# Performance work log

Hardware: AMD Instinct MI355X
Metric: run time of the kernel (lower is better)

## Reference

```python
import jax, jax.numpy as jnp
import numpy as np

D_MODEL = 512
N_HEADS = 8
D_K = 64
D_V = 64
SCALE = 1.0 / np.sqrt(D_K).astype(np.float32)
LN_EPS = 1e-5


def setup_inputs() -> dict:
    key = jax.random.key(0)
    ks = jax.random.split(key, 8)
    B, S = 4, 2048
    xavier = np.sqrt(6.0 / (D_MODEL + D_MODEL)).astype(np.float32)
    return {
        "input_Q": jax.random.normal(ks[0], (B, S, D_MODEL), jnp.float32),
        "input_K": jax.random.normal(ks[1], (B, S, D_MODEL), jnp.float32),
        "input_V": jax.random.normal(ks[2], (B, S, D_MODEL), jnp.float32),
        "attn_mask": jax.random.randint(ks[3], (B, S, S), 0, 2).astype(bool),
        "W_Q": jax.random.uniform(ks[4], (D_MODEL, D_MODEL), jnp.float32, -xavier, xavier),
        "W_K": jax.random.uniform(ks[5], (D_MODEL, D_MODEL), jnp.float32, -xavier, xavier),
        "W_V": jax.random.uniform(ks[6], (D_MODEL, D_MODEL), jnp.float32, -xavier, xavier),
        "W_fc": jax.random.uniform(ks[7], (D_MODEL, D_MODEL), jnp.float32, -xavier, xavier),
        "ln_gamma": jnp.ones((D_MODEL,), jnp.float32),
        "ln_beta": jnp.zeros((D_MODEL,), jnp.float32),
    }


def _layernorm(x, gamma, beta):
    mu = jnp.mean(x, axis=-1, keepdims=True)
    var = jnp.mean(jnp.square(x - mu), axis=-1, keepdims=True)
    return (x - mu) * jax.lax.rsqrt(var + LN_EPS) * gamma + beta


def reference(input_Q, input_K, input_V, attn_mask, W_Q, W_K, W_V, W_fc, ln_gamma, ln_beta):
    B = input_Q.shape[0]
    # torch Linear: x @ W.T ; W is (out, in)
    def proj(x, W):
        y = jnp.einsum('bsd,ed->bse', x, W)  # (B,S,n_heads*d_k)
        return y.reshape(B, -1, N_HEADS, D_K).transpose(0, 2, 1, 3)  # (B,H,S,dk)

    Q = proj(input_Q, W_Q)
    K = proj(input_K, W_K)
    V = proj(input_V, W_V)

    scores = jnp.einsum('bhqd,bhkd->bhqk', Q, K) * SCALE
    scores = jnp.clip(scores, -1e9, 1e10)
    mask = attn_mask[:, None, :, :]  # broadcast over heads
    scores = jnp.where(mask, jnp.float32(-1e9), scores)
    attn = jax.nn.softmax(scores, axis=-1)
    attn = jnp.clip(attn, 1e-8, 1.0)
    result = jnp.einsum('bhqk,bhkd->bhqd', attn, V)
    result = result.transpose(0, 2, 1, 3).reshape(B, -1, N_HEADS * D_V)
    output = jnp.einsum('bsd,ed->bse', result, W_fc)
    out = _layernorm(output + input_Q, ln_gamma, ln_beta)
    return (out, attn)
```

## Files before the change

kernel.cpp:

```cpp
#include <hip/hip_runtime.h>

typedef float  f32x4  __attribute__((ext_vector_type(4)));
typedef __bf16 bf16x8 __attribute__((ext_vector_type(8)));

#define MFMA_BF16(a, b, c) __builtin_amdgcn_mfma_f32_16x16x32_bf16((a), (b), (c), 0, 0, 0)

#define BDIM   4
#define SEQ    2048
#define DM     512
#define NH     8
#define DK     64
#define KT     64
#define NT     (SEQ / KT)
#define QB     128
#define PS     72
#define KTDK   (KT * DK)
#define C2LOG2E  0.18033688011112042f
#define MASKED_X (-115.41560327111707f)

static __device__ __forceinline__ unsigned short f2bf(float f) {
  unsigned int u = __builtin_bit_cast(unsigned int, f);
  u += 0x7fffu + ((u >> 16) & 1u);
  return (unsigned short)(u >> 16);
}
static __device__ __forceinline__ unsigned short rhu(float f) {
  unsigned int u = __builtin_bit_cast(unsigned int, f);
  return (unsigned short)((u + 0x8000u) >> 16);
}
static __device__ __forceinline__ float bf2f(unsigned short u) {
  return __builtin_bit_cast(float, (unsigned)u << 16);
}
static __device__ __forceinline__ float exp2_fast(float x) {
  float r;
  asm("v_exp_f32 %0, %1" : "=v"(r) : "v"(x));
  return r;
}
static __device__ __forceinline__ float log2_fast(float x) {
  float r;
  asm("v_log_f32 %0, %1" : "=v"(r) : "v"(x));
  return r;
}
static __device__ __forceinline__ void gload16(const void* g, unsigned short* l) {
  __builtin_amdgcn_global_load_lds((const __attribute__((address_space(1))) void*)g,
                                   (__attribute__((address_space(3))) void*)l, 16, 0, 0);
}
static __device__ __forceinline__ bf16x8 lds128(const unsigned short* base, int row, int m) {
  return *(const bf16x8*)((const char*)base + row * 128 + (((m) ^ (row & 7)) << 4));
}

__global__ __launch_bounds__(256) void cvt7_kernel(
    const float* __restrict__ x0, const float* __restrict__ x1, const float* __restrict__ x2,
    const float* __restrict__ w0, const float* __restrict__ w1, const float* __restrict__ w2,
    const float* __restrict__ w3,
    unsigned short* __restrict__ dx0, unsigned short* __restrict__ dx1,
    unsigned short* __restrict__ dx2, unsigned short* __restrict__ dw0,
    unsigned short* __restrict__ dw1, unsigned short* __restrict__ dw2,
    unsigned short* __restrict__ dw3, int nx4, int nw4) {
  const int z = blockIdx.y;
  const float* src;
  unsigned short* dst;
  int n4;
  switch (z) {
    case 0: src = x0; dst = dx0; n4 = nx4; break;
    case 1: src = x1; dst = dx1; n4 = nx4; break;
    case 2: src = x2; dst = dx2; n4 = nx4; break;
    case 3: src = w0; dst = dw0; n4 = nw4; break;
    case 4: src = w1; dst = dw1; n4 = nw4; break;
    case 5: src = w2; dst = dw2; n4 = nw4; break;
    default: src = w3; dst = dw3; n4 = nw4; break;
  }
  int i = blockIdx.x * 256 + threadIdx.x;
  if (i >= n4) return;
  float4 v = reinterpret_cast<const float4*>(src)[i];
  ushort4 o;
  o.x = f2bf(v.x); o.y = f2bf(v.y); o.z = f2bf(v.z); o.w = f2bf(v.w);
  reinterpret_cast<ushort4*>(dst)[i] = o;
}

__global__ void detect_mask_kernel(const unsigned int* __restrict__ m, int* __restrict__ flag) {
  __shared__ int s;
  if (threadIdx.x == 0) s = 0;
  __syncthreads();
  int any = 0;
  for (int i = threadIdx.x; i < 4096; i += 256) any |= (m[i] > 1u) ? 1 : 0;
  if (any) atomicOr(&s, 1);
  __syncthreads();
  if (threadIdx.x == 0) *flag = s;
}

__global__ __launch_bounds__(256) void mask_pack_kernel(const unsigned char* __restrict__ m8,
                                                        const int* __restrict__ m32,
                                                        const int* __restrict__ flag,
                                                        unsigned long long* __restrict__ bits) {
  const int wid = blockIdx.x * 256 + threadIdx.x;
  const int use8 = *flag;
  unsigned long long v = 0;
  if (use8) {
    const uchar4* p = (const uchar4*)(m8 + (size_t)wid * 64);
#pragma unroll
    for (int c = 0; c < 16; ++c) {
      uchar4 q = p[c];
      v |= ((unsigned long long)(q.x != 0)) << (c * 4 + 0);
      v |= ((unsigned long long)(q.y != 0)) << (c * 4 + 1);
      v |= ((unsigned long long)(q.z != 0)) << (c * 4 + 2);
      v |= ((unsigned long long)(q.w != 0)) << (c * 4 + 3);
    }
  } else {
    const int4* p = (const int4*)(m32 + (size_t)wid * 64);
#pragma unroll
    for (int c = 0; c < 16; ++c) {
      int4 q = p[c];
      v |= ((unsigned long long)(q.x != 0)) << (c * 4 + 0);
      v |= ((unsigned long long)(q.y != 0)) << (c * 4 + 1);
      v |= ((unsigned long long)(q.z != 0)) << (c * 4 + 2);
      v |= ((unsigned long long)(q.w != 0)) << (c * 4 + 3);
    }
  }
  bits[wid] = v;
}

__device__ __forceinline__ void gemm128_main(const unsigned short* __restrict__ A,
                                             const unsigned short* __restrict__ B,
                                             int K, int row0, int col0,
                                             unsigned short* lds, f32x4 acc[4][4]) {
  const int tid  = threadIdx.x;
  const int w    = tid >> 6;
  const int lane = tid & 63;
  const int lr   = lane & 15;
  const int lk   = (lane >> 4) << 3;
  const int wm   = (w >> 1) << 6;
  const int wn   = (w & 1) << 6;
  unsigned short* As = lds;
  unsigned short* Bs = lds + 128 * 32;
  const int r0 = tid >> 2;
  const int c0 = (tid & 3) << 3;
  const unsigned short* a0 = A + (size_t)(row0 + r0) * K + c0;
  const unsigned short* a1 = A + (size_t)(row0 + r0 + 64) * K + c0;
  const unsigned short* b0 = B + (size_t)(col0 + r0) * K + c0;
  const unsigned short* b1 = B + (size_t)(col0 + r0 + 64) * K + c0;
  unsigned short* dA0 = &As[tid * 8];
  unsigned short* dA1 = &As[(tid + 256) * 8];
  unsigned short* dB0 = &Bs[tid * 8];
  unsigned short* dB1 = &Bs[(tid + 256) * 8];
  for (int k0 = 0; k0 < K; k0 += 32) {
    __syncthreads();
    gload16(a0 + k0, dA0);
    gload16(a1 + k0, dA1);
    gload16(b0 + k0, dB0);
    gload16(b1 + k0, dB1);
    __syncthreads();
    bf16x8 af[4], bfr[4];
#pragma unroll
    for (int mi = 0; mi < 4; ++mi) af[mi]  = *(const bf16x8*)&As[(wm + mi * 16 + lr) * 32 + lk];
#pragma unroll
    for (int ni = 0; ni < 4; ++ni) bfr[ni] = *(const bf16x8*)&Bs[(wn + ni * 16 + lr) * 32 + lk];
#pragma unroll
    for (int mi = 0; mi < 4; ++mi)
#pragma unroll
      for (int ni = 0; ni < 4; ++ni)
        acc[mi][ni] = MFMA_BF16(af[mi], bfr[ni], acc[mi][ni]);
  }
}

__global__ __launch_bounds__(256) void proj_kernel(
    const unsigned short* __restrict__ Xq, const unsigned short* __restrict__ Xk,
    const unsigned short* __restrict__ Xv,
    const unsigned short* __restrict__ Wq, const unsigned short* __restrict__ Wk,
    const unsigned short* __restrict__ Wv,
    unsigned short* __restrict__ Qh, unsigned short* __restrict__ Kh,
    unsigned short* __restrict__ VT) {
  __shared__ __align__(16) unsigned short lds[2 * 128 * 32];
  const int z = blockIdx.z;
  const unsigned short* A = (z == 0) ? Xq : ((z == 1) ? Xk : Xv);
  const unsigned short* B = (z == 0) ? Wq : ((z == 1) ? Wk : Wv);
  unsigned short* O       = (z == 0) ? Qh : ((z == 1) ? Kh : VT);
  const int row0 = blockIdx.x * 128, col0 = blockIdx.y * 128;
  f32x4 acc[4][4];
  const f32x4 zero = {0.f, 0.f, 0.f, 0.f};
#pragma unroll
  for (int mi = 0; mi < 4; ++mi)
#pragma unroll
    for (int ni = 0; ni < 4; ++ni) acc[mi][ni] = zero;
  gemm128_main(A, B, DM, row0, col0, lds, acc);
  const int w = threadIdx.x >> 6, lane = threadIdx.x & 63;
  const int lr = lane & 15, lg = lane >> 4;
  const int wm = (w >> 1) << 6, wn = (w & 1) << 6;
#pragma unroll
  for (int mi = 0; mi < 4; ++mi)
#pragma unroll
    for (int ni = 0; ni < 4; ++ni)
#pragma unroll
      for (int j = 0; j < 4; ++j) {
        const int m = row0 + wm + mi * 16 + lg * 4 + j;
        const int n = col0 + wn + ni * 16 + lr;
        const int b = m >> 11, s = m & 2047;
        const int h = n >> 6,  d = n & 63;
        const unsigned short val = f2bf(acc[mi][ni][j]);
        if (z == 2)
          O[(((size_t)(b * NH + h)) * DK + d) * SEQ + s] = val;
        else
          O[(((size_t)(b * NH + h)) * SEQ + s) * DK + d] = val;
      }
}

__global__ __launch_bounds__(256) void fc_kernel(const unsigned short* __restrict__ A,
                                                 const unsigned short* __restrict__ W,
                                                 float* __restrict__ Out) {
  __shared__ __align__(16) unsigned short lds[2 * 128 * 32];
  const int row0 = blockIdx.x * 128, col0 = blockIdx.y * 128;
  f32x4 acc[4][4];
  const f32x4 zero = {0.f, 0.f, 0.f, 0.f};
#pragma unroll
  for (int mi = 0; mi < 4; ++mi)
#pragma unroll
    for (int ni = 0; ni < 4; ++ni) acc[mi][ni] = zero;
  gemm128_main(A, W, DM, row0, col0, lds, acc);
  const int w = threadIdx.x >> 6, lane = threadIdx.x & 63;
  const int lr = lane & 15, lg = lane >> 4;
  const int wm = (w >> 1) << 6, wn = (w & 1) << 6;
#pragma unroll
  for (int mi = 0; mi < 4; ++mi)
#pragma unroll
    for (int ni = 0; ni < 4; ++ni)
#pragma unroll
      for (int j = 0; j < 4; ++j) {
        const int m = row0 + wm + mi * 16 + lg * 4 + j;
        const int n = col0 + wn + ni * 16 + lr;
        Out[(size_t)m * DM + n] = acc[mi][ni][j];
      }
}

__global__ __launch_bounds__(512, 4) void attn_kernel(
    const unsigned short* __restrict__ Qh, const unsigned short* __restrict__ Kh,
    const unsigned short* __restrict__ VT, const unsigned long long* __restrict__ Mb,
    float* __restrict__ attn_out, unsigned short* __restrict__ R16) {
  __shared__ __align__(16) unsigned short Ks[2][KTDK];
  __shared__ __align__(16) unsigned short Vs[2][KTDK];
  __shared__ __align__(16) unsigned short Pl[8][16 * PS];
  const int id  = blockIdx.x + 16 * (blockIdx.y + 8 * blockIdx.z);
  const int q8  = id >> 3;
  const int bh  = (id & 7) * 4 + (q8 >> 4);
  const int qt  = q8 & 15;
  const int b   = bh >> 3;
  const int tid = threadIdx.x, w = tid >> 6, lane = tid & 63;
  const int lr = lane & 15, lg = lane >> 4;
  const unsigned short* Qp = Qh + (size_t)bh * SEQ * DK;
  const unsigned short* Kp = Kh + (size_t)bh * SEQ * DK;
  const unsigned short* Vp = VT + (size_t)bh * DK * SEQ;
  float* ap = attn_out + (size_t)bh * SEQ * SEQ;

  const int qb = qt * QB + w * 16;
  const bf16x8 qf0 = *(const bf16x8*)(Qp + (size_t)(qb + lr) * DK + lg * 8);
  const bf16x8 qf1 = *(const bf16x8*)(Qp + (size_t)(qb + lr) * DK + 32 + lg * 8);
  const unsigned long long* mrow = Mb + ((size_t)b * SEQ + qb + lr) * 32;

  const int srow = tid >> 3, schunk = tid & 7;
  const int sg = schunk ^ (srow & 7);
  const unsigned short* kstage = Kp + (size_t)srow * DK + sg * 8;
  const unsigned short* vstage = Vp + (size_t)srow * SEQ + sg * 8;
  unsigned short* kdst0 = &Ks[0][tid * 8];
  unsigned short* kdst1 = &Ks[1][tid * 8];
  unsigned short* vdst0 = &Vs[0][tid * 8];
  unsigned short* vdst1 = &Vs[1][tid * 8];

  float l2 = 0.f;
  gload16(kstage, kdst0);
  __syncthreads();
  for (int t = 0; t < NT; ++t) {
    const unsigned short* Kb = Ks[t & 1];
    if (t + 1 < NT) gload16(kstage + (size_t)(t + 1) * KTDK, (t & 1) ? kdst0 : kdst1);
    const unsigned long long mr = mrow[t];
#pragma unroll
    for (int ni = 0; ni < 4; ++ni) {
      const int r = ni * 16 + lr;
      bf16x8 k0 = lds128(Kb, r, lg);
      bf16x8 k1 = lds128(Kb, r, lg + 4);
      f32x4 z = {0.f, 0.f, 0.f, 0.f};
      z = MFMA_BF16(k0, qf0, z);
      z = MFMA_BF16(k1, qf1, z);
#pragma unroll
      for (int j = 0; j < 4; ++j) {
        const float t1 = z[j] * C2LOG2E;
        const float x = ((mr >> (ni * 16 + lg * 4 + j)) & 1ull) ? MASKED_X : t1;
        l2 += exp2_fast(x);
      }
    }
    __syncthreads();
  }
  l2 += __shfl_xor(l2, 16);
  l2 += __shfl_xor(l2, 32);
  const float negllog = -log2_fast(l2);
  const float mAlt = MASKED_X + negllog;

  f32x4 o[4];
  const f32x4 zero = {0.f, 0.f, 0.f, 0.f};
#pragma unroll
  for (int nd = 0; nd < 4; ++nd) o[nd] = zero;
  unsigned short* Pw = &Pl[w][0];

  gload16(kstage, kdst0);
  gload16(vstage, vdst0);
  asm volatile("s_waitcnt vmcnt(0)" ::: "memory");
  __builtin_amdgcn_s_barrier();
  for (int t = 0; t < NT; ++t) {
    const unsigned short* Kb = Ks[t & 1];
    const unsigned short* Vb = Vs[t & 1];
    if (t + 1 < NT) {
      gload16(kstage + (size_t)(t + 1) * KTDK, (t & 1) ? kdst0 : kdst1);
      gload16(vstage + (size_t)(t + 1) * KT,   (t & 1) ? vdst0 : vdst1);
    }
    const unsigned long long mr = mrow[t];
#pragma unroll
    for (int ni = 0; ni < 4; ++ni) {
      const int r = ni * 16 + lr;
      bf16x8 k0 = lds128(Kb, r, lg);
      bf16x8 k1 = lds128(Kb, r, lg + 4);
      f32x4 z = {0.f, 0.f, 0.f, 0.f};
      z = MFMA_BF16(k0, qf0, z);
      z = MFMA_BF16(k1, qf1, z);
      float p[4];
#pragma unroll
      for (int j = 0; j < 4; ++j) {
        const float t1 = fmaf(z[j], C2LOG2E, negllog);
        const float x = ((mr >> (ni * 16 + lg * 4 + j)) & 1ull) ? mAlt : t1;
        p[j] = exp2_fast(x);
      }
      ushort4 pk = {rhu(p[0]), rhu(p[1]), rhu(p[2]), rhu(p[3])};
      *(ushort4*)&Pw[lr * PS + ni * 16 + lg * 4] = pk;
    }
    const bf16x8 pf0 = *(const bf16x8*)&Pw[lr * PS + lg * 8];
    const bf16x8 pf1 = *(const bf16x8*)&Pw[lr * PS + 32 + lg * 8];
#pragma unroll
    for (int nd = 0; nd < 4; ++nd) {
      const int r = nd * 16 + lr;
      o[nd] = MFMA_BF16(pf0, lds128(Vb, r, lg), o[nd]);
    }
#pragma unroll
    for (int nd = 0; nd < 4; ++nd) {
      const int r = nd * 16 + lr;
      o[nd] = MFMA_BF16(pf1, lds128(Vb, r, lg + 4), o[nd]);
    }
#pragma unroll
    for (int j = 0; j < 4; ++j) {
      const int r = lg * 4 + j;
      ushort4 pk = *(const ushort4*)&Pw[r * PS + lr * 4];
      float4 f = {bf2f(pk.x), bf2f(pk.y), bf2f(pk.z), bf2f(pk.w)};
      *(float4*)(ap + (size_t)(qb + r) * SEQ + t * KT + lr * 4) = f;
    }
    if (t + 1 < NT) {
      asm volatile("s_waitcnt vmcnt(4)" ::: "memory");
      __builtin_amdgcn_s_barrier();
    }
  }
#pragma unroll
  for (int nd = 0; nd < 4; ++nd)
#pragma unroll
    for (int j = 0; j < 4; ++j)
      R16[((size_t)(b * SEQ + qb + lg * 4 + j)) * DM + (bh & 7) * DK + nd * 16 + lr] = f2bf(o[nd][j]);
}

__global__ __launch_bounds__(256) void ln_kernel(const float* __restrict__ fc,
                                                 const float* __restrict__ xq,
                                                 const float* __restrict__ gamma,
                                                 const float* __restrict__ beta,
                                                 float* __restrict__ out) {
  const int row = blockIdx.x * 4 + (threadIdx.x >> 6);
  const int lane = threadIdx.x & 63;
  const float* f = fc + (size_t)row * DM;
  const float* x = xq + (size_t)row * DM;
  float v[8];
  float s = 0.f, ss = 0.f;
#pragma unroll
  for (int i = 0; i < 8; ++i) {
    const int c = lane + i * 64;
    const float t = f[c] + x[c];
    v[i] = t; s += t; ss += t * t;
  }
#pragma unroll
  for (int off = 1; off < 64; off <<= 1) {
    s  += __shfl_xor(s, off);
    ss += __shfl_xor(ss, off);
  }
  const float mu  = s * (1.f / 512.f);
  const float var = ss * (1.f / 512.f) - mu * mu;
  const float inv = rsqrtf(var + 1e-5f);
  float* op = out + (size_t)row * DM;
#pragma unroll
  for (int i = 0; i < 8; ++i) {
    const int c = lane + i * 64;
    op[c] = (v[i] - mu) * inv * gamma[c] + beta[c];
  }
}


extern "C" void kernel_launch(void* const* d_in, const int* in_sizes, int n_in,
                              void* d_out, int out_size, void* d_ws, size_t ws_size,
                              hipStream_t stream) {
  const float* xq   = (const float*)d_in[0];
  const float* xk   = (const float*)d_in[1];
  const float* xv   = (const float*)d_in[2];
  const void*  mask = d_in[3];
  const float* wq   = (const float*)d_in[4];
  const float* wk   = (const float*)d_in[5];
  const float* wv   = (const float*)d_in[6];
  const float* wfc  = (const float*)d_in[7];
  const float* gamma = (const float*)d_in[8];
  const float* beta  = (const float*)d_in[9];

  float* out = (float*)d_out;
  float* attn_out = out + (size_t)BDIM * SEQ * DM;

  char* ws = (char*)d_ws;
  unsigned short* XQ16 = (unsigned short*)(ws);
  unsigned short* XK16 = (unsigned short*)(ws + 8388608);
  unsigned short* XV16 = (unsigned short*)(ws + 16777216);
  unsigned short* WQ16 = (unsigned short*)(ws + 25165824);
  unsigned short* WK16 = (unsigned short*)(ws + 25690112);
  unsigned short* WV16 = (unsigned short*)(ws + 26214400);
  unsigned short* WF16 = (unsigned short*)(ws + 26738688);
  unsigned short* Qh   = (unsigned short*)(ws + 27262976);
  unsigned short* Kh   = (unsigned short*)(ws + 35651584);
  unsigned short* VT   = (unsigned short*)(ws + 44040192);
  unsigned long long* Mbits = (unsigned long long*)(ws);
  unsigned short* R16  = (unsigned short*)(ws + 16777216);
  float*          FC32 = (float*)(ws + 27262976);
  int*            FLAG = (int*)(ws + 52428800);

  const int NX4 = BDIM * SEQ * DM / 4;
  const int NW4 = DM * DM / 4;

  detect_mask_kernel<<<1, 256, 0, stream>>>((const unsigned int*)mask, FLAG);
  cvt7_kernel<<<dim3(NX4 / 256, 7), 256, 0, stream>>>(xq, xk, xv, wq, wk, wv, wfc,
                                                      XQ16, XK16, XV16,
                                                      WQ16, WK16, WV16, WF16, NX4, NW4);
  proj_kernel<<<dim3(64, 4, 3), 256, 0, stream>>>(XQ16, XK16, XV16,
                                                  WQ16, WK16, WV16, Qh, Kh, VT);
  mask_pack_kernel<<<1024, 256, 0, stream>>>((const unsigned char*)mask,
                                             (const int*)mask, FLAG, Mbits);
  attn_kernel<<<dim3(16, NH, BDIM), 512, 0, stream>>>(Qh, Kh, VT, Mbits, attn_out, R16);
  fc_kernel<<<dim3(64, 4, 1), 256, 0, stream>>>(R16, WF16, FC32);
  ln_kernel<<<2048, 256, 0, stream>>>(FC32, xq, gamma, beta, out);
}
```

Measured before the change: 305.0 us.

## Give each attention wave two query row tiles to reuse K/V LDS fragments

The attention block shrinks from 8 waves to 4, and each wave now handles two 16-row query tiles (A and B). Every K and V fragment read from LDS feeds two MFMAs, so LDS reads per MFMA are halved. Each thread stages two 16-byte chunks per tile, and the vmcnt wait goes from 4 to 8 to match the extra loads. In exchange, registers per wave roughly double and there are fewer waves per block to hide latency, with launch bounds set to 256 threads and 3 blocks per CU.

```diff
diff --git a/kernel.cpp b/kernel.cpp
--- a/kernel.cpp
+++ b/kernel.cpp
@@ -230,13 +230,13 @@
       }
 }
 
-__global__ __launch_bounds__(512, 4) void attn_kernel(
+__global__ __launch_bounds__(256, 3) void attn_kernel(
     const unsigned short* __restrict__ Qh, const unsigned short* __restrict__ Kh,
     const unsigned short* __restrict__ VT, const unsigned long long* __restrict__ Mb,
     float* __restrict__ attn_out, unsigned short* __restrict__ R16) {
   __shared__ __align__(16) unsigned short Ks[2][KTDK];
   __shared__ __align__(16) unsigned short Vs[2][KTDK];
-  __shared__ __align__(16) unsigned short Pl[8][16 * PS];
+  __shared__ __align__(16) unsigned short Pl[4][2][16 * PS];
   const int id  = blockIdx.x + 16 * (blockIdx.y + 8 * blockIdx.z);
   const int q8  = id >> 3;
   const int bh  = (id & 7) * 4 + (q8 >> 4);
@@ -249,114 +249,151 @@
   const unsigned short* Vp = VT + (size_t)bh * DK * SEQ;
   float* ap = attn_out + (size_t)bh * SEQ * SEQ;
 
-  const int qb = qt * QB + w * 16;
-  const bf16x8 qf0 = *(const bf16x8*)(Qp + (size_t)(qb + lr) * DK + lg * 8);
-  const bf16x8 qf1 = *(const bf16x8*)(Qp + (size_t)(qb + lr) * DK + 32 + lg * 8);
-  const unsigned long long* mrow = Mb + ((size_t)b * SEQ + qb + lr) * 32;
-
-  const int srow = tid >> 3, schunk = tid & 7;
-  const int sg = schunk ^ (srow & 7);
-  const unsigned short* kstage = Kp + (size_t)srow * DK + sg * 8;
-  const unsigned short* vstage = Vp + (size_t)srow * SEQ + sg * 8;
-  unsigned short* kdst0 = &Ks[0][tid * 8];
-  unsigned short* kdst1 = &Ks[1][tid * 8];
-  unsigned short* vdst0 = &Vs[0][tid * 8];
-  unsigned short* vdst1 = &Vs[1][tid * 8];
-
-  float l2 = 0.f;
-  gload16(kstage, kdst0);
+  const int qbA = qt * QB + w * 32;
+  const int qbB = qbA + 16;
+  const bf16x8 qfA0 = *(const bf16x8*)(Qp + (size_t)(qbA + lr) * DK + lg * 8);
+  const bf16x8 qfA1 = *(const bf16x8*)(Qp + (size_t)(qbA + lr) * DK + 32 + lg * 8);
+  const bf16x8 qfB0 = *(const bf16x8*)(Qp + (size_t)(qbB + lr) * DK + lg * 8);
+  const bf16x8 qfB1 = *(const bf16x8*)(Qp + (size_t)(qbB + lr) * DK + 32 + lg * 8);
+  const unsigned long long* mrowA = Mb + ((size_t)b * SEQ + qbA + lr) * 32;
+  const unsigned long long* mrowB = Mb + ((size_t)b * SEQ + qbB + lr) * 32;
+
+  const int ci0 = tid, ci1 = tid + 256;
+  const int sr0 = ci0 >> 3, sc0 = (ci0 & 7) ^ (sr0 & 7);
+  const int sr1 = ci1 >> 3, sc1 = (ci1 & 7) ^ (sr1 & 7);
+  const unsigned short* kst0 = Kp + (size_t)sr0 * DK + sc0 * 8;
+  const unsigned short* kst1 = Kp + (size_t)sr1 * DK + sc1 * 8;
+  const unsigned short* vst0 = Vp + (size_t)sr0 * SEQ + sc0 * 8;
+  const unsigned short* vst1 = Vp + (size_t)sr1 * SEQ + sc1 * 8;
+
+  float l2A = 0.f, l2B = 0.f;
+  gload16(kst0, &Ks[0][ci0 * 8]);
+  gload16(kst1, &Ks[0][ci1 * 8]);
   __syncthreads();
   for (int t = 0; t < NT; ++t) {
     const unsigned short* Kb = Ks[t & 1];
-    if (t + 1 < NT) gload16(kstage + (size_t)(t + 1) * KTDK, (t & 1) ? kdst0 : kdst1);
-    const unsigned long long mr = mrow[t];
+    if (t + 1 < NT) {
+      gload16(kst0 + (size_t)(t + 1) * KTDK, &Ks[(t & 1) ^ 1][ci0 * 8]);
+      gload16(kst1 + (size_t)(t + 1) * KTDK, &Ks[(t & 1) ^ 1][ci1 * 8]);
+    }
+    const unsigned long long mrA = mrowA[t];
+    const unsigned long long mrB = mrowB[t];
 #pragma unroll
     for (int ni = 0; ni < 4; ++ni) {
       const int r = ni * 16 + lr;
       bf16x8 k0 = lds128(Kb, r, lg);
       bf16x8 k1 = lds128(Kb, r, lg + 4);
-      f32x4 z = {0.f, 0.f, 0.f, 0.f};
-      z = MFMA_BF16(k0, qf0, z);
-      z = MFMA_BF16(k1, qf1, z);
+      f32x4 zA = {0.f, 0.f, 0.f, 0.f};
+      zA = MFMA_BF16(k0, qfA0, zA);
+      zA = MFMA_BF16(k1, qfA1, zA);
+      f32x4 zB = {0.f, 0.f, 0.f, 0.f};
+      zB = MFMA_BF16(k0, qfB0, zB);
+      zB = MFMA_BF16(k1, qfB1, zB);
 #pragma unroll
       for (int j = 0; j < 4; ++j) {
-        const float t1 = z[j] * C2LOG2E;
-        const float x = ((mr >> (ni * 16 + lg * 4 + j)) & 1ull) ? MASKED_X : t1;
-        l2 += exp2_fast(x);
+        const int bit = ni * 16 + lg * 4 + j;
+        const float xA = ((mrA >> bit) & 1ull) ? MASKED_X : zA[j] * C2LOG2E;
+        const float xB = ((mrB >> bit) & 1ull) ? MASKED_X : zB[j] * C2LOG2E;
+        l2A += exp2_fast(xA);
+        l2B += exp2_fast(xB);
       }
     }
     __syncthreads();
   }
-  l2 += __shfl_xor(l2, 16);
-  l2 += __shfl_xor(l2, 32);
-  const float negllog = -log2_fast(l2);
-  const float mAlt = MASKED_X + negllog;
-
-  f32x4 o[4];
+  l2A += __shfl_xor(l2A, 16);
+  l2A += __shfl_xor(l2A, 32);
+  l2B += __shfl_xor(l2B, 16);
+  l2B += __shfl_xor(l2B, 32);
+  const float negllogA = -log2_fast(l2A);
+  const float negllogB = -log2_fast(l2B);
+  const float mAltA = MASKED_X + negllogA;
+  const float mAltB = MASKED_X + negllogB;
+
+  f32x4 oA[4], oB[4];
   const f32x4 zero = {0.f, 0.f, 0.f, 0.f};
 #pragma unroll
-  for (int nd = 0; nd < 4; ++nd) o[nd] = zero;
-  unsigned short* Pw = &Pl[w][0];
-
-  gload16(kstage, kdst0);
-  gload16(vstage, vdst0);
+  for (int nd = 0; nd < 4; ++nd) { oA[nd] = zero; oB[nd] = zero; }
+  unsigned short* PwA = &Pl[w][0][0];
+  unsigned short* PwB = &Pl[w][1][0];
+
+  gload16(kst0, &Ks[0][ci0 * 8]);
+  gload16(kst1, &Ks[0][ci1 * 8]);
+  gload16(vst0, &Vs[0][ci0 * 8]);
+  gload16(vst1, &Vs[0][ci1 * 8]);
   asm volatile("s_waitcnt vmcnt(0)" ::: "memory");
   __builtin_amdgcn_s_barrier();
   for (int t = 0; t < NT; ++t) {
     const unsigned short* Kb = Ks[t & 1];
     const unsigned short* Vb = Vs[t & 1];
     if (t + 1 < NT) {
-      gload16(kstage + (size_t)(t + 1) * KTDK, (t & 1) ? kdst0 : kdst1);
-      gload16(vstage + (size_t)(t + 1) * KT,   (t & 1) ? vdst0 : vdst1);
-    }
-    const unsigned long long mr = mrow[t];
+      gload16(kst0 + (size_t)(t + 1) * KTDK, &Ks[(t & 1) ^ 1][ci0 * 8]);
+      gload16(kst1 + (size_t)(t + 1) * KTDK, &Ks[(t & 1) ^ 1][ci1 * 8]);
+      gload16(vst0 + (size_t)(t + 1) * KT,   &Vs[(t & 1) ^ 1][ci0 * 8]);
+      gload16(vst1 + (size_t)(t + 1) * KT,   &Vs[(t & 1) ^ 1][ci1 * 8]);
+    }
+    const unsigned long long mrA = mrowA[t];
+    const unsigned long long mrB = mrowB[t];
 #pragma unroll
     for (int ni = 0; ni < 4; ++ni) {
       const int r = ni * 16 + lr;
       bf16x8 k0 = lds128(Kb, r, lg);
       bf16x8 k1 = lds128(Kb, r, lg + 4);
-      f32x4 z = {0.f, 0.f, 0.f, 0.f};
-      z = MFMA_BF16(k0, qf0, z);
-      z = MFMA_BF16(k1, qf1, z);
-      float p[4];
+      f32x4 zA = {0.f, 0.f, 0.f, 0.f};
+      zA = MFMA_BF16(k0, qfA0, zA);
+      zA = MFMA_BF16(k1, qfA1, zA);
+      f32x4 zB = {0.f, 0.f, 0.f, 0.f};
+      zB = MFMA_BF16(k0, qfB0, zB);
+      zB = MFMA_BF16(k1, qfB1, zB);
+      float pA[4], pB[4];
 #pragma unroll
       for (int j = 0; j < 4; ++j) {
-        const float t1 = fmaf(z[j], C2LOG2E, negllog);
-        const float x = ((mr >> (ni * 16 + lg * 4 + j)) & 1ull) ? mAlt : t1;
-        p[j] = exp2_fast(x);
+        const int bit = ni * 16 + lg * 4 + j;
+        const float xA = ((mrA >> bit) & 1ull) ? mAltA : fmaf(zA[j], C2LOG2E, negllogA);
+        const float xB = ((mrB >> bit) & 1ull) ? mAltB : fmaf(zB[j], C2LOG2E, negllogB);
+        pA[j] = exp2_fast(xA);
+        pB[j] = exp2_fast(xB);
       }
-      ushort4 pk = {rhu(p[0]), rhu(p[1]), rhu(p[2]), rhu(p[3])};
-      *(ushort4*)&Pw[lr * PS + ni * 16 + lg * 4] = pk;
-    }
-    const bf16x8 pf0 = *(const bf16x8*)&Pw[lr * PS + lg * 8];
-    const bf16x8 pf1 = *(const bf16x8*)&Pw[lr * PS + 32 + lg * 8];
+      ushort4 pkA = {rhu(pA[0]), rhu(pA[1]), rhu(pA[2]), rhu(pA[3])};
+      ushort4 pkB = {rhu(pB[0]), rhu(pB[1]), rhu(pB[2]), rhu(pB[3])};
+      *(ushort4*)&PwA[lr * PS + ni * 16 + lg * 4] = pkA;
+      *(ushort4*)&PwB[lr * PS + ni * 16 + lg * 4] = pkB;
+    }
+    const bf16x8 pfA0 = *(const bf16x8*)&PwA[lr * PS + lg * 8];
+    const bf16x8 pfA1 = *(const bf16x8*)&PwA[lr * PS + 32 + lg * 8];
+    const bf16x8 pfB0 = *(const bf16x8*)&PwB[lr * PS + lg * 8];
+    const bf16x8 pfB1 = *(const bf16x8*)&PwB[lr * PS + 32 + lg * 8];
 #pragma unroll
     for (int nd = 0; nd < 4; ++nd) {
       const int r = nd * 16 + lr;
-      o[nd] = MFMA_BF16(pf0, lds128(Vb, r, lg), o[nd]);
-    }
-#pragma unroll
-    for (int nd = 0; nd < 4; ++nd) {
-      const int r = nd * 16 + lr;
-      o[nd] = MFMA_BF16(pf1, lds128(Vb, r, lg + 4), o[nd]);
+      bf16x8 v0 = lds128(Vb, r, lg);
+      bf16x8 v1 = lds128(Vb, r, lg + 4);
+      oA[nd] = MFMA_BF16(pfA0, v0, oA[nd]);
+      oA[nd] = MFMA_BF16(pfA1, v1, oA[nd]);
+      oB[nd] = MFMA_BF16(pfB0, v0, oB[nd]);
+      oB[nd] = MFMA_BF16(pfB1, v1, oB[nd]);
     }
 #pragma unroll
     for (int j = 0; j < 4; ++j) {
       const int r = lg * 4 + j;
-      ushort4 pk = *(const ushort4*)&Pw[r * PS + lr * 4];
-      float4 f = {bf2f(pk.x), bf2f(pk.y), bf2f(pk.z), bf2f(pk.w)};
-      *(float4*)(ap + (size_t)(qb + r) * SEQ + t * KT + lr * 4) = f;
+      ushort4 pkA = *(const ushort4*)&PwA[r * PS + lr * 4];
+      float4 fA = {bf2f(pkA.x), bf2f(pkA.y), bf2f(pkA.z), bf2f(pkA.w)};
+      *(float4*)(ap + (size_t)(qbA + r) * SEQ + t * KT + lr * 4) = fA;
+      ushort4 pkB = *(const ushort4*)&PwB[r * PS + lr * 4];
+      float4 fB = {bf2f(pkB.x), bf2f(pkB.y), bf2f(pkB.z), bf2f(pkB.w)};
+      *(float4*)(ap + (size_t)(qbB + r) * SEQ + t * KT + lr * 4) = fB;
     }
     if (t + 1 < NT) {
-      asm volatile("s_waitcnt vmcnt(4)" ::: "memory");
+      asm volatile("s_waitcnt vmcnt(8)" ::: "memory");
       __builtin_amdgcn_s_barrier();
     }
   }
 #pragma unroll
   for (int nd = 0; nd < 4; ++nd)
 #pragma unroll
-    for (int j = 0; j < 4; ++j)
-      R16[((size_t)(b * SEQ + qb + lg * 4 + j)) * DM + (bh & 7) * DK + nd * 16 + lr] = f2bf(o[nd][j]);
+    for (int j = 0; j < 4; ++j) {
+      R16[((size_t)(b * SEQ + qbA + lg * 4 + j)) * DM + (bh & 7) * DK + nd * 16 + lr] = f2bf(oA[nd][j]);
+      R16[((size_t)(b * SEQ + qbB + lg * 4 + j)) * DM + (bh & 7) * DK + nd * 16 + lr] = f2bf(oB[nd][j]);
+    }
 }
 
 __global__ __launch_bounds__(256) void ln_kernel(const float* __restrict__ fc,
@@ -437,7 +474,7 @@
                                                   WQ16, WK16, WV16, Qh, Kh, VT);
   mask_pack_kernel<<<1024, 256, 0, stream>>>((const unsigned char*)mask,
                                              (const int*)mask, FLAG, Mbits);
-  attn_kernel<<<dim3(16, NH, BDIM), 512, 0, stream>>>(Qh, Kh, VT, Mbits, attn_out, R16);
+  attn_kernel<<<dim3(16, NH, BDIM), 256, 0, stream>>>(Qh, Kh, VT, Mbits, attn_out, R16);
   fc_kernel<<<dim3(64, 4, 1), 256, 0, stream>>>(R16, WF16, FC32);
   ln_kernel<<<2048, 256, 0, stream>>>(FC32, xq, gamma, beta, out);
 }
```

Measured after the change: 305.0 us. No clear change (+0.0%).
